# Optimization experiments

Measured on AMD Instinct MI355X. Metric: run time of the kernel, lower is better.

The kernel has to match this reference:

```python
import jax, jax.numpy as jnp
import numpy as np


def setup_inputs() -> dict:
    key = jax.random.key(0)
    k1, k2 = jax.random.split(key)
    B, T, D, K = 8, 4096, 256, 1024
    z = jax.random.normal(k1, (B, T, D), dtype=jnp.float32)
    codebook = jax.random.uniform(k2, (K, D), dtype=jnp.float32)
    return {"z": z, "codebook": codebook}


def reference(z, codebook):
    # Squared L2 distance via dot-product decomposition (same argmin as
    # the broadcasted squared-difference in the original module, without
    # materializing the (B,T,K,D) intermediate).
    #   ||z - c||^2 = ||z||^2 - 2 z.c + ||c||^2
    z_sq = jnp.sum(z * z, axis=-1, keepdims=True)            # (B,T,1)
    c_sq = jnp.sum(codebook * codebook, axis=-1)             # (K,)
    cross = jnp.einsum("btd,kd->btk", z, codebook)           # (B,T,K)
    l2_distance = z_sq - 2.0 * cross + c_sq                  # (B,T,K)
    codebook_indices = jnp.argmin(l2_distance, axis=-1)      # (B,T)
    z_q = codebook[codebook_indices]                         # (B,T,D)
    # Straight-through estimator
    z_q = z + jax.lax.stop_gradient(z_q - z)
    return (z_q, codebook_indices)
```

## Files before the change

### kernel.cpp

```cpp
#include <hip/hip_runtime.h>
#include <math.h>

#define NTOK   32768
#define NDIM   256
#define NCODE  1024

#define TM 128
#define TN 128
#define KC 32
#define NTILES (NCODE / TN)
#define CHUNK  (128 * KC)

typedef _Float16 f16x8 __attribute__((ext_vector_type(8)));
typedef float    f32x4 __attribute__((ext_vector_type(4)));

__device__ __forceinline__ void gld_lds16(const void* g, void* l) {
    __builtin_amdgcn_global_load_lds(
        (const __attribute__((address_space(1))) void*)g,
        (__attribute__((address_space(3))) void*)l, 16, 0, 0);
}

__global__ __launch_bounds__(256) void prep_split(
        const float* __restrict__ z, const float* __restrict__ cb,
        _Float16* __restrict__ zh, _Float16* __restrict__ zl,
        _Float16* __restrict__ ch, _Float16* __restrict__ cl,
        float* __restrict__ csq) {
    const bool is_cb = blockIdx.x >= 4096;
    const int  bb    = is_cb ? (blockIdx.x - 4096) : blockIdx.x;
    const int  L     = bb * 256 + threadIdx.x;
    const int  row   = L >> 5;
    const int  g     = L & 31;

    const float* src = (is_cb ? cb : z) + (size_t)row * NDIM + g * 8;
    float4 a0 = *(const float4*)src;
    float4 a1 = *(const float4*)(src + 4);
    float v[8] = {a0.x, a0.y, a0.z, a0.w, a1.x, a1.y, a1.z, a1.w};
    f16x8 hi, lo;
    float s = 0.f;
    #pragma unroll
    for (int e = 0; e < 8; ++e) {
        _Float16 h = (_Float16)v[e];
        hi[e] = h;
        lo[e] = (_Float16)(v[e] - (float)h);
        s += v[e] * v[e];
    }
    const int rb = row >> 7, r = row & 127, kc8 = g >> 2, k8 = g & 3;
    const size_t dst = (size_t)(rb * 8 + kc8) * CHUNK + r * KC + k8 * 8;
    if (is_cb) {
        *(f16x8*)&ch[dst] = hi;
        *(f16x8*)&cl[dst] = lo;
        #pragma unroll
        for (int off = 16; off > 0; off >>= 1) s += __shfl_down(s, off, 32);
        if ((threadIdx.x & 31) == 0) csq[row] = s;
    } else {
        *(f16x8*)&zh[dst] = hi;
        *(f16x8*)&zl[dst] = lo;
    }
}

__global__ __launch_bounds__(256, 4) void vq_mfma_argmin(
        const _Float16* __restrict__ zh, const _Float16* __restrict__ zl,
        const _Float16* __restrict__ ch, const _Float16* __restrict__ cl,
        const float* __restrict__ csq,
        float2* __restrict__ pq) {
    __shared__ _Float16 Ah[TM * KC];
    __shared__ _Float16 Al[TM * KC];
    __shared__ _Float16 Bh[TN * KC];
    __shared__ _Float16 Bl[TN * KC];

    const int tid    = threadIdx.x;
    const int nstrip = blockIdx.x;
    const int mblk   = blockIdx.y;
    const int n0     = nstrip * TN;
    const int wave   = tid >> 6;
    const int lane   = tid & 63;
    const int wy = wave >> 1, wx = wave & 1;
    const int quad = lane >> 4, lr = lane & 15;

    const _Float16* gsrc;
    _Float16* ldst;
    if      (wave == 0) { gsrc = zh + (size_t)mblk * (8 * CHUNK); ldst = Ah; }
    else if (wave == 1) { gsrc = zl + (size_t)mblk * (8 * CHUNK); ldst = Al; }
    else if (wave == 2) { gsrc = ch + (size_t)nstrip * (8 * CHUNK); ldst = Bh; }
    else                { gsrc = cl + (size_t)nstrip * (8 * CHUNK); ldst = Bl; }
    gsrc += lane * 8;

    f32x4 acc[4][4];
    #pragma unroll
    for (int i = 0; i < 4; ++i)
        #pragma unroll
        for (int j = 0; j < 4; ++j) acc[i][j] = (f32x4){0.f, 0.f, 0.f, 0.f};

    for (int kc8 = 0; kc8 < 8; ++kc8) {
        __syncthreads();
        #pragma unroll
        for (int j = 0; j < 8; ++j)
            gld_lds16(gsrc + kc8 * CHUNK + j * 512, ldst + j * 512);
        __syncthreads();

        f16x8 fah[4], fal[4], fbh[4], fbl[4];
        #pragma unroll
        for (int t = 0; t < 4; ++t) {
            int aoff = (wy * 64 + t * 16 + lr) * KC + quad * 8;
            int boff = (wx * 64 + t * 16 + lr) * KC + quad * 8;
            fah[t] = *(const f16x8*)&Ah[aoff];
            fal[t] = *(const f16x8*)&Al[aoff];
            fbh[t] = *(const f16x8*)&Bh[boff];
            fbl[t] = *(const f16x8*)&Bl[boff];
        }
        #pragma unroll
        for (int mt = 0; mt < 4; ++mt)
            #pragma unroll
            for (int nt = 0; nt < 4; ++nt) {
                acc[mt][nt] = __builtin_amdgcn_mfma_f32_16x16x32_f16(
                                  fah[mt], fbh[nt], acc[mt][nt], 0, 0, 0);
                acc[mt][nt] = __builtin_amdgcn_mfma_f32_16x16x32_f16(
                                  fal[mt], fbh[nt], acc[mt][nt], 0, 0, 0);
                acc[mt][nt] = __builtin_amdgcn_mfma_f32_16x16x32_f16(
                                  fah[mt], fbl[nt], acc[mt][nt], 0, 0, 0);
            }
    }

    float cs[4];
    #pragma unroll
    for (int nt = 0; nt < 4; ++nt) cs[nt] = csq[n0 + wx * 64 + nt * 16 + lr];

    __syncthreads();
    float* cv = (float*)Ah;
    int*   ci = (int*)Bh;

    #pragma unroll
    for (int mt = 0; mt < 4; ++mt)
        #pragma unroll
        for (int r = 0; r < 4; ++r) {
            float bv = INFINITY; int bi = 0x7fffffff;
            #pragma unroll
            for (int nt = 0; nt < 4; ++nt) {
                float v = cs[nt] - 2.0f * acc[mt][nt][r];
                int   n = n0 + wx * 64 + nt * 16 + lr;
                if (v < bv || (v == bv && n < bi)) { bv = v; bi = n; }
            }
            #pragma unroll
            for (int msk = 1; msk < 16; msk <<= 1) {
                float ov = __shfl_xor(bv, msk, 64);
                int   oi = __shfl_xor(bi, msk, 64);
                if (ov < bv || (ov == bv && oi < bi)) { bv = ov; bi = oi; }
            }
            if (lr == 0) {
                int ml = wy * 64 + mt * 16 + quad * 4 + r;
                cv[ml * 2 + wx] = bv;
                ci[ml * 2 + wx] = bi;
            }
        }
    __syncthreads();

    if (tid < TM) {
        float v0 = cv[tid * 2], v1 = cv[tid * 2 + 1];
        int   i0 = ci[tid * 2], i1 = ci[tid * 2 + 1];
        bool take1 = (v1 < v0) || (v1 == v0 && i1 < i0);
        int token = mblk * TM + tid;
        pq[(size_t)token * NTILES + nstrip] =
            make_float2(take1 ? v1 : v0, __int_as_float(take1 ? i1 : i0));
    }
}

__global__ __launch_bounds__(256) void vq_finalize(
        const float2* __restrict__ pq, const float* __restrict__ cb,
        float* __restrict__ zq, float* __restrict__ io) {
    __shared__ int best[16];
    const int tid = threadIdx.x;
    const int t0 = blockIdx.x * 16;

    if (tid < 16) {
        int token = t0 + tid;
        float bv = INFINITY; int bi = 0x7fffffff;
        #pragma unroll
        for (int j = 0; j < NTILES; ++j) {
            float2 p = pq[(size_t)token * NTILES + j];
            int i = __float_as_int(p.y);
            if (p.x < bv || (p.x == bv && i < bi)) { bv = p.x; bi = i; }
        }
        best[tid] = bi;
        io[token] = (float)bi;
    }
    __syncthreads();

    const int tr = tid >> 4, tc = tid & 15;
    const float* src = cb + (size_t)best[tr] * NDIM;
    float*       dst = zq + (size_t)(t0 + tr) * NDIM;
    #pragma unroll
    for (int q = 0; q < 4; ++q) {
        int col = q * 64 + tc * 4;
        *(float4*)&dst[col] = *(const float4*)&src[col];
    }
}

extern "C" void kernel_launch(void* const* d_in, const int* in_sizes, int n_in,
                              void* d_out, int out_size, void* d_ws, size_t ws_size,
                              hipStream_t stream) {
    const float* z  = (const float*)d_in[0];
    const float* cb = (const float*)d_in[1];

    float* zq = (float*)d_out;
    float* io = (float*)d_out + (size_t)NTOK * NDIM;

    _Float16* zh = (_Float16*)d_out;
    _Float16* zl = zh + (size_t)NTOK * NDIM;

    _Float16* ch  = (_Float16*)d_ws;
    _Float16* cl  = ch + (size_t)NCODE * NDIM;
    float*    csq = (float*)(cl + (size_t)NCODE * NDIM);
    float2*   pq  = (float2*)(csq + NCODE);

    prep_split<<<4096 + 128, 256, 0, stream>>>(z, cb, zh, zl, ch, cl, csq);

    dim3 grid(NTILES, NTOK / TM);
    vq_mfma_argmin<<<grid, 256, 0, stream>>>(zh, zl, ch, cl, csq, pq);

    vq_finalize<<<NTOK / 16, 256, 0, stream>>>(pq, cb, zq, io);
}
```

Before: 158.1 us.

## Stage prep split through LDS for coalesced stores and remap GEMM block order

The prep kernel now has each block process 64 rows in groups of 8. The fp16 hi/lo halves are staged in padded shared memory so the global stores into the tiled chunk layout are written in contiguous 16-byte runs rather than scattered. The main MFMA kernel switches to a 1D grid with a swizzled mapping that groups 8 token blocks with all 8 codebook strips, aiming for better L2 reuse. The cost is extra syncthreads and fewer, longer-running prep blocks.

```diff
diff --git a/kernel.cpp b/kernel.cpp
--- a/kernel.cpp
+++ b/kernel.cpp
@@ -20,41 +20,66 @@
         (__attribute__((address_space(3))) void*)l, 16, 0, 0);
 }
 
+#define SLDS 264
 __global__ __launch_bounds__(256) void prep_split(
         const float* __restrict__ z, const float* __restrict__ cb,
         _Float16* __restrict__ zh, _Float16* __restrict__ zl,
         _Float16* __restrict__ ch, _Float16* __restrict__ cl,
         float* __restrict__ csq) {
-    const bool is_cb = blockIdx.x >= 4096;
-    const int  bb    = is_cb ? (blockIdx.x - 4096) : blockIdx.x;
-    const int  L     = bb * 256 + threadIdx.x;
-    const int  row   = L >> 5;
-    const int  g     = L & 31;
-
-    const float* src = (is_cb ? cb : z) + (size_t)row * NDIM + g * 8;
-    float4 a0 = *(const float4*)src;
-    float4 a1 = *(const float4*)(src + 4);
-    float v[8] = {a0.x, a0.y, a0.z, a0.w, a1.x, a1.y, a1.z, a1.w};
-    f16x8 hi, lo;
-    float s = 0.f;
-    #pragma unroll
-    for (int e = 0; e < 8; ++e) {
-        _Float16 h = (_Float16)v[e];
-        hi[e] = h;
-        lo[e] = (_Float16)(v[e] - (float)h);
-        s += v[e] * v[e];
-    }
-    const int rb = row >> 7, r = row & 127, kc8 = g >> 2, k8 = g & 3;
-    const size_t dst = (size_t)(rb * 8 + kc8) * CHUNK + r * KC + k8 * 8;
-    if (is_cb) {
-        *(f16x8*)&ch[dst] = hi;
-        *(f16x8*)&cl[dst] = lo;
-        #pragma unroll
-        for (int off = 16; off > 0; off >>= 1) s += __shfl_down(s, off, 32);
-        if ((threadIdx.x & 31) == 0) csq[row] = s;
-    } else {
-        *(f16x8*)&zh[dst] = hi;
-        *(f16x8*)&zl[dst] = lo;
+    __shared__ _Float16 Hs[8 * SLDS];
+    __shared__ _Float16 Ls[8 * SLDS];
+
+    const bool is_cb = blockIdx.x >= 512;
+    const int  blk   = is_cb ? (blockIdx.x - 512) : blockIdx.x;
+    const int  row0  = blk * 64;
+    const float* src = (is_cb ? cb : z) + (size_t)row0 * NDIM;
+    _Float16* ph = is_cb ? ch : zh;
+    _Float16* pl = is_cb ? cl : zl;
+    const int t = threadIdx.x;
+
+    for (int grp = 0; grp < 8; ++grp) {
+        const int r = t >> 5;
+        const int g = t & 31;
+        const float* p = src + ((size_t)(grp * 8 + r) * NDIM + g * 8);
+        float4 a0 = *(const float4*)p;
+        float4 a1 = *(const float4*)(p + 4);
+        float v[8] = {a0.x, a0.y, a0.z, a0.w, a1.x, a1.y, a1.z, a1.w};
+        f16x8 hi, lo;
+        float s = 0.f;
+        #pragma unroll
+        for (int e = 0; e < 8; ++e) {
+            _Float16 h = (_Float16)v[e];
+            hi[e] = h;
+            lo[e] = (_Float16)(v[e] - (float)h);
+            s += v[e] * v[e];
+        }
+        if (grp) __syncthreads();
+        *(f16x8*)&Hs[r * SLDS + g * 8] = hi;
+        *(f16x8*)&Ls[r * SLDS + g * 8] = lo;
+        if (is_cb) {
+            #pragma unroll
+            for (int off = 16; off > 0; off >>= 1) s += __shfl_down(s, off, 32);
+            if ((t & 31) == 0) csq[row0 + grp * 8 + r] = s;
+        }
+        __syncthreads();
+
+        const int rowbase = row0 + grp * 8;
+        const int rb = rowbase >> 7;
+        const int rr0 = rowbase & 127;
+        #pragma unroll
+        for (int io2 = 0; io2 < 2; ++io2) {
+            int t2   = t + io2 * 256;
+            int kc8  = t2 >> 6;
+            int pls  = (t2 >> 5) & 1;
+            int slot = t2 & 31;
+            int r2   = slot >> 2;
+            int q    = slot & 3;
+            const _Float16* S = pls ? Ls : Hs;
+            f16x8 w = *(const f16x8*)&S[r2 * SLDS + kc8 * 32 + q * 8];
+            _Float16* D = pls ? pl : ph;
+            size_t dst = (size_t)(rb * 8 + kc8) * CHUNK + (rr0 + r2) * KC + q * 8;
+            *(f16x8*)&D[dst] = w;
+        }
     }
 }
 
@@ -68,9 +93,12 @@
     __shared__ _Float16 Bh[TN * KC];
     __shared__ _Float16 Bl[TN * KC];
 
-    const int tid    = threadIdx.x;
-    const int nstrip = blockIdx.x;
-    const int mblk   = blockIdx.y;
+    const int tid = threadIdx.x;
+    const int lin = blockIdx.x;
+    const int x      = lin & 7;
+    const int j      = lin >> 3;
+    const int nstrip = j & 7;
+    const int mblk   = ((j >> 3) << 3) | x;
     const int n0     = nstrip * TN;
     const int wave   = tid >> 6;
     const int lane   = tid & 63;
@@ -89,13 +117,13 @@
     #pragma unroll
     for (int i = 0; i < 4; ++i)
         #pragma unroll
-        for (int j = 0; j < 4; ++j) acc[i][j] = (f32x4){0.f, 0.f, 0.f, 0.f};
+        for (int j2 = 0; j2 < 4; ++j2) acc[i][j2] = (f32x4){0.f, 0.f, 0.f, 0.f};
 
     for (int kc8 = 0; kc8 < 8; ++kc8) {
         __syncthreads();
         #pragma unroll
-        for (int j = 0; j < 8; ++j)
-            gld_lds16(gsrc + kc8 * CHUNK + j * 512, ldst + j * 512);
+        for (int j2 = 0; j2 < 8; ++j2)
+            gld_lds16(gsrc + kc8 * CHUNK + j2 * 512, ldst + j2 * 512);
         __syncthreads();
 
         f16x8 fah[4], fal[4], fbh[4], fbl[4];
@@ -212,10 +240,10 @@
     float*    csq = (float*)(cl + (size_t)NCODE * NDIM);
     float2*   pq  = (float2*)(csq + NCODE);
 
-    prep_split<<<4096 + 128, 256, 0, stream>>>(z, cb, zh, zl, ch, cl, csq);
-
-    dim3 grid(NTILES, NTOK / TM);
-    vq_mfma_argmin<<<grid, 256, 0, stream>>>(zh, zl, ch, cl, csq, pq);
+    prep_split<<<512 + 16, 256, 0, stream>>>(z, cb, zh, zl, ch, cl, csq);
+
+    vq_mfma_argmin<<<NTILES * (NTOK / TM), 256, 0, stream>>>(
+        zh, zl, ch, cl, csq, pq);
 
     vq_finalize<<<NTOK / 16, 256, 0, stream>>>(pq, cb, zq, io);
 }
```

New measurement: 155.4 us. No clear change (-1.7%).

## Fuse z split, GEMM argmin, and gather into one kernel with register-resident z

Applied to the files above, without the earlier changes.

Removes the separate z fp16 hi/lo split pass and the partial-argmin/finalize kernels. Each block now owns 64 tokens, converts z to fp16 hi/lo directly in registers, and loops over all 8 codebook strips, keeping a running argmin before gathering codebook rows into the output. The aim is to cut the global traffic of z splits and partial results and to drop kernel launches. In exchange there are fewer, larger blocks (512), each re-streaming the whole codebook through LDS with synchronous loads and no double buffering. Register pressure is also higher.

```diff
diff --git a/kernel.cpp b/kernel.cpp
--- a/kernel.cpp
+++ b/kernel.cpp
@@ -4,12 +4,8 @@
 #define NTOK   32768
 #define NDIM   256
 #define NCODE  1024
-
-#define TM 128
-#define TN 128
-#define KC 32
-#define NTILES (NCODE / TN)
-#define CHUNK  (128 * KC)
+#define NSTRIP 8
+#define CHUNK  (128 * 32)
 
 typedef _Float16 f16x8 __attribute__((ext_vector_type(8)));
 typedef float    f32x4 __attribute__((ext_vector_type(4)));
@@ -20,18 +16,15 @@
         (__attribute__((address_space(3))) void*)l, 16, 0, 0);
 }
 
-__global__ __launch_bounds__(256) void prep_split(
-        const float* __restrict__ z, const float* __restrict__ cb,
-        _Float16* __restrict__ zh, _Float16* __restrict__ zl,
+__global__ __launch_bounds__(256) void prep_cb(
+        const float* __restrict__ cb,
         _Float16* __restrict__ ch, _Float16* __restrict__ cl,
         float* __restrict__ csq) {
-    const bool is_cb = blockIdx.x >= 4096;
-    const int  bb    = is_cb ? (blockIdx.x - 4096) : blockIdx.x;
-    const int  L     = bb * 256 + threadIdx.x;
-    const int  row   = L >> 5;
-    const int  g     = L & 31;
+    const int L   = blockIdx.x * 256 + threadIdx.x;
+    const int row = L >> 5;
+    const int g   = L & 31;
 
-    const float* src = (is_cb ? cb : z) + (size_t)row * NDIM + g * 8;
+    const float* src = cb + (size_t)row * NDIM + g * 8;
     float4 a0 = *(const float4*)src;
     float4 a1 = *(const float4*)(src + 4);
     float v[8] = {a0.x, a0.y, a0.z, a0.w, a1.x, a1.y, a1.z, a1.w};
@@ -44,154 +37,143 @@
         lo[e] = (_Float16)(v[e] - (float)h);
         s += v[e] * v[e];
     }
-    const int rb = row >> 7, r = row & 127, kc8 = g >> 2, k8 = g & 3;
-    const size_t dst = (size_t)(rb * 8 + kc8) * CHUNK + r * KC + k8 * 8;
-    if (is_cb) {
-        *(f16x8*)&ch[dst] = hi;
-        *(f16x8*)&cl[dst] = lo;
-        #pragma unroll
-        for (int off = 16; off > 0; off >>= 1) s += __shfl_down(s, off, 32);
-        if ((threadIdx.x & 31) == 0) csq[row] = s;
-    } else {
-        *(f16x8*)&zh[dst] = hi;
-        *(f16x8*)&zl[dst] = lo;
-    }
+    const size_t dst = (size_t)((row >> 7) * 8 + (g >> 2)) * CHUNK
+                     + (row & 127) * 32 + (g & 3) * 8;
+    *(f16x8*)&ch[dst] = hi;
+    *(f16x8*)&cl[dst] = lo;
+    #pragma unroll
+    for (int off = 16; off > 0; off >>= 1) s += __shfl_down(s, off, 32);
+    if ((threadIdx.x & 31) == 0) csq[row] = s;
 }
 
-__global__ __launch_bounds__(256, 4) void vq_mfma_argmin(
-        const _Float16* __restrict__ zh, const _Float16* __restrict__ zl,
+__global__ __launch_bounds__(256, 2) void vq_main(
+        const float* __restrict__ z,
         const _Float16* __restrict__ ch, const _Float16* __restrict__ cl,
-        const float* __restrict__ csq,
-        float2* __restrict__ pq) {
-    __shared__ _Float16 Ah[TM * KC];
-    __shared__ _Float16 Al[TM * KC];
-    __shared__ _Float16 Bh[TN * KC];
-    __shared__ _Float16 Bl[TN * KC];
+        const float* __restrict__ csq, const float* __restrict__ cb,
+        float* __restrict__ zq, float* __restrict__ io) {
+    __shared__ _Float16 Bh[4 * CHUNK];
+    __shared__ _Float16 Bl[4 * CHUNK];
 
-    const int tid    = threadIdx.x;
-    const int nstrip = blockIdx.x;
-    const int mblk   = blockIdx.y;
-    const int n0     = nstrip * TN;
-    const int wave   = tid >> 6;
-    const int lane   = tid & 63;
-    const int wy = wave >> 1, wx = wave & 1;
+    const int tid  = threadIdx.x;
+    const int w    = tid >> 6;
+    const int lane = tid & 63;
     const int quad = lane >> 4, lr = lane & 15;
+    const int m0   = blockIdx.x * 64;
 
-    const _Float16* gsrc;
-    _Float16* ldst;
-    if      (wave == 0) { gsrc = zh + (size_t)mblk * (8 * CHUNK); ldst = Ah; }
-    else if (wave == 1) { gsrc = zl + (size_t)mblk * (8 * CHUNK); ldst = Al; }
-    else if (wave == 2) { gsrc = ch + (size_t)nstrip * (8 * CHUNK); ldst = Bh; }
-    else                { gsrc = cl + (size_t)nstrip * (8 * CHUNK); ldst = Bl; }
-    gsrc += lane * 8;
-
-    f32x4 acc[4][4];
-    #pragma unroll
-    for (int i = 0; i < 4; ++i)
+    f16x8 ah[8], al[8];
+    {
+        const float* zp = z + (size_t)(m0 + w * 16 + lr) * NDIM + quad * 8;
         #pragma unroll
-        for (int j = 0; j < 4; ++j) acc[i][j] = (f32x4){0.f, 0.f, 0.f, 0.f};
-
-    for (int kc8 = 0; kc8 < 8; ++kc8) {
-        __syncthreads();
-        #pragma unroll
-        for (int j = 0; j < 8; ++j)
-            gld_lds16(gsrc + kc8 * CHUNK + j * 512, ldst + j * 512);
-        __syncthreads();
-
-        f16x8 fah[4], fal[4], fbh[4], fbl[4];
-        #pragma unroll
-        for (int t = 0; t < 4; ++t) {
-            int aoff = (wy * 64 + t * 16 + lr) * KC + quad * 8;
-            int boff = (wx * 64 + t * 16 + lr) * KC + quad * 8;
-            fah[t] = *(const f16x8*)&Ah[aoff];
-            fal[t] = *(const f16x8*)&Al[aoff];
-            fbh[t] = *(const f16x8*)&Bh[boff];
-            fbl[t] = *(const f16x8*)&Bl[boff];
+        for (int c = 0; c < 8; ++c) {
+            float4 a0 = *(const float4*)(zp + c * 32);
+            float4 a1 = *(const float4*)(zp + c * 32 + 4);
+            float v[8] = {a0.x, a0.y, a0.z, a0.w, a1.x, a1.y, a1.z, a1.w};
+            #pragma unroll
+            for (int e = 0; e < 8; ++e) {
+                _Float16 h = (_Float16)v[e];
+                ah[c][e] = h;
+                al[c][e] = (_Float16)(v[e] - (float)h);
+            }
         }
-        #pragma unroll
-        for (int mt = 0; mt < 4; ++mt)
-            #pragma unroll
-            for (int nt = 0; nt < 4; ++nt) {
-                acc[mt][nt] = __builtin_amdgcn_mfma_f32_16x16x32_f16(
-                                  fah[mt], fbh[nt], acc[mt][nt], 0, 0, 0);
-                acc[mt][nt] = __builtin_amdgcn_mfma_f32_16x16x32_f16(
-                                  fal[mt], fbh[nt], acc[mt][nt], 0, 0, 0);
-                acc[mt][nt] = __builtin_amdgcn_mfma_f32_16x16x32_f16(
-                                  fah[mt], fbl[nt], acc[mt][nt], 0, 0, 0);
-            }
     }
 
-    float cs[4];
+    float bv[4];
+    int   bi[4];
     #pragma unroll
-    for (int nt = 0; nt < 4; ++nt) cs[nt] = csq[n0 + wx * 64 + nt * 16 + lr];
+    for (int r = 0; r < 4; ++r) { bv[r] = INFINITY; bi[r] = 0x7fffffff; }
+
+    f32x4 acc[8];
+    #pragma unroll
+    for (int nt = 0; nt < 8; ++nt) acc[nt] = (f32x4){0.f, 0.f, 0.f, 0.f};
+
+    for (int strip = 0; strip < NSTRIP; ++strip) {
+        float cs[8];
+        #pragma unroll
+        for (int nt = 0; nt < 8; ++nt)
+            cs[nt] = csq[strip * 128 + nt * 16 + lr];
+
+        #pragma unroll
+        for (int kh = 0; kh < 2; ++kh) {
+            __syncthreads();
+            {
+                const size_t base = (size_t)(strip * 8 + kh * 4) * CHUNK
+                                  + w * CHUNK + lane * 8;
+                const _Float16* sh = ch + base;
+                const _Float16* sl = cl + base;
+                #pragma unroll
+                for (int i = 0; i < 8; ++i) {
+                    gld_lds16(sh + i * 512, Bh + w * CHUNK + i * 512);
+                    gld_lds16(sl + i * 512, Bl + w * CHUNK + i * 512);
+                }
+            }
+            __syncthreads();
+
+            #pragma unroll
+            for (int k4 = 0; k4 < 4; ++k4) {
+                const int kg = kh * 4 + k4;
+                f16x8 fbh[8], fbl[8];
+                #pragma unroll
+                for (int nt = 0; nt < 8; ++nt) {
+                    const int off = k4 * CHUNK + (nt * 16 + lr) * 32 + quad * 8;
+                    fbh[nt] = *(const f16x8*)&Bh[off];
+                    fbl[nt] = *(const f16x8*)&Bl[off];
+                }
+                #pragma unroll
+                for (int nt = 0; nt < 8; ++nt) {
+                    acc[nt] = __builtin_amdgcn_mfma_f32_16x16x32_f16(
+                                  ah[kg], fbh[nt], acc[nt], 0, 0, 0);
+                    acc[nt] = __builtin_amdgcn_mfma_f32_16x16x32_f16(
+                                  al[kg], fbh[nt], acc[nt], 0, 0, 0);
+                    acc[nt] = __builtin_amdgcn_mfma_f32_16x16x32_f16(
+                                  ah[kg], fbl[nt], acc[nt], 0, 0, 0);
+                }
+            }
+        }
+
+        #pragma unroll
+        for (int r = 0; r < 4; ++r)
+            #pragma unroll
+            for (int nt = 0; nt < 8; ++nt) {
+                float v = cs[nt] - 2.0f * acc[nt][r];
+                int   n = strip * 128 + nt * 16 + lr;
+                if (v < bv[r] || (v == bv[r] && n < bi[r])) { bv[r] = v; bi[r] = n; }
+            }
+        #pragma unroll
+        for (int nt = 0; nt < 8; ++nt) acc[nt] = (f32x4){0.f, 0.f, 0.f, 0.f};
+    }
+
+    #pragma unroll
+    for (int msk = 1; msk < 16; msk <<= 1)
+        #pragma unroll
+        for (int r = 0; r < 4; ++r) {
+            float ov = __shfl_xor(bv[r], msk, 64);
+            int   oi = __shfl_xor(bi[r], msk, 64);
+            if (ov < bv[r] || (ov == bv[r] && oi < bi[r])) { bv[r] = ov; bi[r] = oi; }
+        }
 
     __syncthreads();
-    float* cv = (float*)Ah;
-    int*   ci = (int*)Bh;
-
-    #pragma unroll
-    for (int mt = 0; mt < 4; ++mt)
+    int* bestS = (int*)Bh;
+    if (lr == 0) {
         #pragma unroll
         for (int r = 0; r < 4; ++r) {
-            float bv = INFINITY; int bi = 0x7fffffff;
-            #pragma unroll
-            for (int nt = 0; nt < 4; ++nt) {
-                float v = cs[nt] - 2.0f * acc[mt][nt][r];
-                int   n = n0 + wx * 64 + nt * 16 + lr;
-                if (v < bv || (v == bv && n < bi)) { bv = v; bi = n; }
-            }
-            #pragma unroll
-            for (int msk = 1; msk < 16; msk <<= 1) {
-                float ov = __shfl_xor(bv, msk, 64);
-                int   oi = __shfl_xor(bi, msk, 64);
-                if (ov < bv || (ov == bv && oi < bi)) { bv = ov; bi = oi; }
-            }
-            if (lr == 0) {
-                int ml = wy * 64 + mt * 16 + quad * 4 + r;
-                cv[ml * 2 + wx] = bv;
-                ci[ml * 2 + wx] = bi;
-            }
+            int row = w * 16 + quad * 4 + r;
+            bestS[row] = bi[r];
+            io[m0 + row] = (float)bi[r];
         }
-    __syncthreads();
-
-    if (tid < TM) {
-        float v0 = cv[tid * 2], v1 = cv[tid * 2 + 1];
-        int   i0 = ci[tid * 2], i1 = ci[tid * 2 + 1];
-        bool take1 = (v1 < v0) || (v1 == v0 && i1 < i0);
-        int token = mblk * TM + tid;
-        pq[(size_t)token * NTILES + nstrip] =
-            make_float2(take1 ? v1 : v0, __int_as_float(take1 ? i1 : i0));
-    }
-}
-
-__global__ __launch_bounds__(256) void vq_finalize(
-        const float2* __restrict__ pq, const float* __restrict__ cb,
-        float* __restrict__ zq, float* __restrict__ io) {
-    __shared__ int best[16];
-    const int tid = threadIdx.x;
-    const int t0 = blockIdx.x * 16;
-
-    if (tid < 16) {
-        int token = t0 + tid;
-        float bv = INFINITY; int bi = 0x7fffffff;
-        #pragma unroll
-        for (int j = 0; j < NTILES; ++j) {
-            float2 p = pq[(size_t)token * NTILES + j];
-            int i = __float_as_int(p.y);
-            if (p.x < bv || (p.x == bv && i < bi)) { bv = p.x; bi = i; }
-        }
-        best[tid] = bi;
-        io[token] = (float)bi;
     }
     __syncthreads();
 
     const int tr = tid >> 4, tc = tid & 15;
-    const float* src = cb + (size_t)best[tr] * NDIM;
-    float*       dst = zq + (size_t)(t0 + tr) * NDIM;
     #pragma unroll
-    for (int q = 0; q < 4; ++q) {
-        int col = q * 64 + tc * 4;
-        *(float4*)&dst[col] = *(const float4*)&src[col];
+    for (int p = 0; p < 4; ++p) {
+        int row = p * 16 + tr;
+        const float* src = cb + (size_t)bestS[row] * NDIM;
+        float*       dst = zq + (size_t)(m0 + row) * NDIM;
+        #pragma unroll
+        for (int q = 0; q < 4; ++q) {
+            int col = q * 64 + tc * 4;
+            *(float4*)&dst[col] = *(const float4*)&src[col];
+        }
     }
 }
 
@@ -204,18 +186,11 @@
     float* zq = (float*)d_out;
     float* io = (float*)d_out + (size_t)NTOK * NDIM;
 
-    _Float16* zh = (_Float16*)d_out;
-    _Float16* zl = zh + (size_t)NTOK * NDIM;
-
     _Float16* ch  = (_Float16*)d_ws;
     _Float16* cl  = ch + (size_t)NCODE * NDIM;
     float*    csq = (float*)(cl + (size_t)NCODE * NDIM);
-    float2*   pq  = (float2*)(csq + NCODE);
 
-    prep_split<<<4096 + 128, 256, 0, stream>>>(z, cb, zh, zl, ch, cl, csq);
+    prep_cb<<<NCODE * 32 / 256, 256, 0, stream>>>(cb, ch, cl, csq);
 
-    dim3 grid(NTILES, NTOK / TM);
-    vq_mfma_argmin<<<grid, 256, 0, stream>>>(zh, zl, ch, cl, csq, pq);
-
-    vq_finalize<<<NTOK / 16, 256, 0, stream>>>(pq, cb, zq, io);
+    vq_main<<<NTOK / 64, 256, 0, stream>>>(z, ch, cl, csq, cb, zq, io);
 }
```

Result: faster. 139.7 us (-11.6%).
